# Kernel tuning notes

Measured on AMD Instinct MI355X. Metric: run time of the kernel, lower is better.

## Reference

```python
import jax, jax.numpy as jnp
import numpy as np

B = 32768  # batch of 8x8 boards
DIRS = ((0, 1), (1, 0), (1, 1), (1, -1))  # row, col, main diag, anti diag


def _shift(m, di, dj):
    # out[b,i,j] = m[b,i-di,j-dj], zeros outside the board
    H, W = m.shape[-2], m.shape[-1]
    p = jnp.pad(m, ((0, 0), (max(di, 0), max(-di, 0)), (max(dj, 0), max(-dj, 0))))
    a, b = max(-di, 0), max(-dj, 0)
    return p[:, a:a + H, b:b + W]


def _run_length(m, di, dj):
    # length of the maximal run of ones through each cell along direction (di,dj); 0 where m==0
    left = m
    p = m
    for k in range(1, 8):
        p = p * _shift(m, k * di, k * dj)
        left = left + p
    right = m
    p = m
    for k in range(1, 8):
        p = p * _shift(m, -k * di, -k * dj)
        right = right + p
    return left + right - m


def _conn_channels(m, Ns):
    runs = [_run_length(m, di, dj) for di, dj in DIRS]
    out = []
    for N in Ns:
        c = jnp.zeros(m.shape, dtype=bool)
        for r in runs:
            c = c | (r == N)
        out.append(c.astype(m.dtype))
    return out


def _mark(arr, cond, k0, width):
    u = jnp.broadcast_to(cond[..., None].astype(arr.dtype), cond.shape + (width,))
    return arr.at[..., k0:k0 + width].max(u)


def _line_features(me, op, empty):
    # me/op: [B,R,8] float {0,1}; empty: [B,R,8] bool; lines along last axis
    live2 = jnp.zeros_like(me)
    live3 = jnp.zeros_like(me)
    rush3 = jnp.zeros_like(me)

    def blocked(idx):
        if idx < 0 or idx > 7:  # off-board counts as blocked
            return jnp.ones(me.shape[:-1], dtype=bool)
        return (op[..., idx] > 0) | ((~empty[..., idx]) & (me[..., idx] == 0))

    for k in range(5):  # length-4 windows
        a = ((me[..., k] > 0) & (me[..., k + 1] > 0) & (me[..., k + 2] == 0)
             & (me[..., k + 3] == 0) & empty[..., k + 2] & empty[..., k + 3])
        live2 = _mark(live2, a, k, 2)
        b = ((me[..., k] == 0) & (me[..., k + 1] > 0) & (me[..., k + 2] > 0)
             & (me[..., k + 3] == 0) & empty[..., k] & empty[..., k + 3])
        live2 = _mark(live2, b, k + 1, 2)
    for k in range(4):  # length-5 windows
        open3 = ((me[..., k] == 0) & (me[..., k + 1] > 0) & (me[..., k + 2] > 0)
                 & (me[..., k + 3] > 0) & (me[..., k + 4] == 0))
        c = open3 & empty[..., k] & empty[..., k + 4]
        live3 = _mark(live3, c, k + 1, 3)
        lb, rb = blocked(k - 1), blocked(k + 5)
        d = ((me[..., k] > 0) & (me[..., k + 1] > 0) & (me[..., k + 2] > 0)
             & (me[..., k + 3] == 0) & (me[..., k + 4] == 0) & empty[..., k + 3] & lb)
        rush3 = _mark(rush3, d, k, 3)
        e = open3 & jnp.logical_xor(lb, rb)
        rush3 = _mark(rush3, e, k + 1, 3)
    return live2, live3, rush3


def _live_rush(me, op):
    empty = (me == 0) & (op == 0)
    l2r, l3r, r3r = _line_features(me, op, empty)  # rows
    T = lambda x: jnp.swapaxes(x, 1, 2)
    l2c, l3c, r3c = _line_features(T(me), T(op), T(empty))  # cols
    return (jnp.maximum(l2r, T(l2c)), jnp.maximum(l3r, T(l3c)), jnp.maximum(r3r, T(r3c)))


def _double(x, threshold=2):
    cnt = jnp.sum(x, axis=(1, 2), keepdims=True)
    return (cnt >= threshold).astype(x.dtype) * jnp.ones_like(x)


def setup_inputs() -> dict:
    key = jax.random.key(0)
    k1, _ = jax.random.split(key)
    state = jax.random.randint(k1, (B, 8, 8), 0, 3).astype(jnp.float32) - 1.0  # {-1,0,1}
    side = jnp.ones((B,), dtype=jnp.float32)
    return {"state": state, "side": side}


def reference(state, side):
    s = side[:, None, None]
    my = (state == s).astype(jnp.float32)
    op = (state == -s).astype(jnp.float32)
    feats = [my, op]
    feats += _conn_channels(my, [1, 2, 3])
    feats += _conn_channels(op, [1, 2, 3])
    l2m, l3m, r3m = _live_rush(my, op)
    l2o, l3o, r3o = _live_rush(op, my)
    feats += [l2m, l3m, r3m, _double(l2m, 2), _double(l3m + r3m, 2)]
    feats += [l2o, l3o, r3o, _double(l2o, 2), _double(l3o + r3o, 2)]
    return jnp.stack(feats, axis=1)  # [B, 18, 8, 8]
```

## Files before the change

### kernel.cpp

```cpp
#include <hip/hip_runtime.h>

typedef unsigned long long u64;

#define FILE0 0x0101010101010101ULL
#define NF0   0xFEFEFEFEFEFEFEFEULL
#define NF7   0x7F7F7F7F7F7F7F7FULL

template<int D> __device__ __forceinline__ u64 SH(u64 x) {
  if (D == 0) return (x << 1) & NF0;
  if (D == 1) return x << 8;
  if (D == 2) return (x << 9) & NF0;
  return (x << 7) & NF7;
}
template<int D> __device__ __forceinline__ u64 FW(u64 x) {
  if (D == 0) return (x >> 1) & NF7;
  if (D == 1) return x >> 8;
  if (D == 2) return (x >> 9) & NF7;
  return (x >> 7) & NF0;
}

template<int D> __device__ __forceinline__ void runs(u64 b, u64& r1, u64& r2, u64& r3) {
  u64 f1 = FW<D>(b), f2 = FW<D>(f1), f3 = FW<D>(f2);
  u64 start = b & ~SH<D>(b);
  r1 |= start & ~f1;
  u64 st2 = start & f1 & ~f2;
  r2 |= st2 | SH<D>(st2);
  u64 st3 = start & f1 & f2 & ~f3;
  u64 s3a = SH<D>(st3);
  r3 |= st3 | s3a | SH<D>(s3a);
}

template<int D> __device__ __forceinline__ void linefeat(u64 me, u64 op, u64 empty,
                                                         u64& live2, u64& live3, u64& rush3) {
  const u64 EDGE_LO  = (D == 0) ? FILE0 : 0xFFULL;
  const u64 EDGE_HI3 = (D == 0) ? 0xF8F8F8F8F8F8F8F8ULL
                                : 0xFFFFFFFFFF000000ULL;
  u64 fm1 = FW<D>(me), fm2 = FW<D>(fm1), fm3 = FW<D>(fm2);
  u64 fe1 = FW<D>(empty), fe2 = FW<D>(fe1), fe3 = FW<D>(fe2), fe4 = FW<D>(fe3);
  u64 fn4 = FW<D>(FW<D>(FW<D>(FW<D>(~me))));
  u64 a = me & fm1 & fe2 & fe3;
  live2 |= a | SH<D>(a);
  u64 b = empty & fm1 & fm2 & fe3;
  u64 sb = SH<D>(b);
  live2 |= sb | SH<D>(sb);
  u64 c = empty & fm1 & fm2 & fm3 & fe4;
  u64 sc = SH<D>(c), sc2 = SH<D>(sc);
  live3 |= sc | sc2 | SH<D>(sc2);
  u64 lb  = SH<D>(op) | EDGE_LO;
  u64 fo5 = FW<D>(FW<D>(FW<D>(FW<D>(FW<D>(op)))));
  u64 rb  = fo5 | EDGE_HI3;
  u64 open3 = (~me) & fm1 & fm2 & fm3 & fn4;
  u64 e = open3 & (lb ^ rb);
  u64 se = SH<D>(e), se2 = SH<D>(se);
  rush3 |= se | se2 | SH<D>(se2);
  u64 d = me & fm1 & fm2 & fe3 & fn4 & lb;
  u64 sd = SH<D>(d);
  rush3 |= d | sd | SH<D>(sd);
}

__global__ __launch_bounds__(256) void Agent_56822417326533_kernel(
    const float* __restrict__ state, const float* __restrict__ side,
    float* __restrict__ out, int B) {
  const int lane = threadIdx.x & 63;
  const int wave = blockIdx.x * (blockDim.x >> 6) + (threadIdx.x >> 6);
  const int board0 = wave * 8;
  if (board0 >= B) return;

  u64 my = 0, op = 0;
  const float* sp = state + (size_t)board0 * 64;
  #pragma unroll
  for (int j = 0; j < 8; ++j) {
    if (board0 + j < B) {
      float s = side[board0 + j];
      float v = sp[j * 64 + lane];
      u64 mym = __ballot(v == s);
      u64 opm = __ballot(v == -s);
      if (lane == j) { my = mym; op = opm; }
    }
  }

  u64 empty = ~(my | op);
  u64 ch[18];
  ch[0] = my; ch[1] = op;

  u64 r1m = 0, r2m = 0, r3m = 0, r1o = 0, r2o = 0, r3o = 0;
  runs<0>(my, r1m, r2m, r3m); runs<1>(my, r1m, r2m, r3m);
  runs<2>(my, r1m, r2m, r3m); runs<3>(my, r1m, r2m, r3m);
  runs<0>(op, r1o, r2o, r3o); runs<1>(op, r1o, r2o, r3o);
  runs<2>(op, r1o, r2o, r3o); runs<3>(op, r1o, r2o, r3o);
  ch[2] = r1m; ch[3] = r2m; ch[4] = r3m;
  ch[5] = r1o; ch[6] = r2o; ch[7] = r3o;

  u64 l2m = 0, l3m = 0, ru3m = 0, l2o = 0, l3o = 0, ru3o = 0;
  linefeat<0>(my, op, empty, l2m, l3m, ru3m);
  linefeat<1>(my, op, empty, l2m, l3m, ru3m);
  linefeat<0>(op, my, empty, l2o, l3o, ru3o);
  linefeat<1>(op, my, empty, l2o, l3o, ru3o);
  ch[8] = l2m; ch[9] = l3m; ch[10] = ru3m;
  ch[11] = (__popcll(l2m) >= 2) ? ~0ULL : 0ULL;
  ch[12] = (__popcll(l3m) + __popcll(ru3m) >= 2) ? ~0ULL : 0ULL;
  ch[13] = l2o; ch[14] = l3o; ch[15] = ru3o;
  ch[16] = (__popcll(l2o) >= 2) ? ~0ULL : 0ULL;
  ch[17] = (__popcll(l3o) + __popcll(ru3o) >= 2) ? ~0ULL : 0ULL;

  float* outp = out + (size_t)board0 * 1152 + lane;
  #pragma unroll
  for (int j = 0; j < 8; ++j) {
    if (board0 + j < B) {
      #pragma unroll
      for (int c = 0; c < 18; ++c) {
        u64 m = __shfl(ch[c], j);
        outp[j * 1152 + c * 64] = (float)((m >> lane) & 1ULL);
      }
    }
  }
}

extern "C" void kernel_launch(void* const* d_in, const int* in_sizes, int n_in,
                              void* d_out, int out_size, void* d_ws, size_t ws_size,
                              hipStream_t stream) {
  const float* state = (const float*)d_in[0];
  const float* side  = (const float*)d_in[1];
  float* out = (float*)d_out;
  const int B = in_sizes[0] / 64;
  const int boards_per_block = 32;
  const int blocks = (B + boards_per_block - 1) / boards_per_block;
  hipLaunchKernelGGL(Agent_56822417326533_kernel, dim3(blocks), dim3(256), 0, stream,
                     state, side, out, B);
}
```

Baseline: 159.5 us.

## Process one board per wave and store channels as vectorized float4 writes

Each wave now handles a single board instead of eight. The whole wave computes the bitboard features redundantly, so the per-lane board gather and the 144 shuffles per wave are no longer needed. The output is written with float4 stores (four channels per pass via lane-group selection) plus a float2 tail, which cuts the number of store instructions. In exchange the launch has eight times more waves, and every lane repeats the same scalar bit arithmetic.

```diff
diff --git a/kernel.cpp b/kernel.cpp
--- a/kernel.cpp
+++ b/kernel.cpp
@@ -38,6 +38,7 @@
   u64 fm1 = FW<D>(me), fm2 = FW<D>(fm1), fm3 = FW<D>(fm2);
   u64 fe1 = FW<D>(empty), fe2 = FW<D>(fe1), fe3 = FW<D>(fe2), fe4 = FW<D>(fe3);
   u64 fn4 = FW<D>(FW<D>(FW<D>(FW<D>(~me))));
+  (void)fe1;
   u64 a = me & fm1 & fe2 & fe3;
   live2 |= a | SH<D>(a);
   u64 b = empty & fm1 & fm2 & fe3;
@@ -58,28 +59,25 @@
   rush3 |= d | sd | SH<D>(sd);
 }
 
+__device__ __forceinline__ u64 sel4(int idx, u64 a, u64 b, u64 c, u64 d) {
+  u64 ab = (idx & 1) ? b : a;
+  u64 cd = (idx & 1) ? d : c;
+  return (idx & 2) ? cd : ab;
+}
+
 __global__ __launch_bounds__(256) void Agent_56822417326533_kernel(
     const float* __restrict__ state, const float* __restrict__ side,
     float* __restrict__ out, int B) {
   const int lane = threadIdx.x & 63;
-  const int wave = blockIdx.x * (blockDim.x >> 6) + (threadIdx.x >> 6);
-  const int board0 = wave * 8;
-  if (board0 >= B) return;
+  const int board = blockIdx.x * 4 + (threadIdx.x >> 6);
+  if (board >= B) return;
 
-  u64 my = 0, op = 0;
-  const float* sp = state + (size_t)board0 * 64;
-  #pragma unroll
-  for (int j = 0; j < 8; ++j) {
-    if (board0 + j < B) {
-      float s = side[board0 + j];
-      float v = sp[j * 64 + lane];
-      u64 mym = __ballot(v == s);
-      u64 opm = __ballot(v == -s);
-      if (lane == j) { my = mym; op = opm; }
-    }
-  }
+  const float s = side[board];
+  const float v = state[(size_t)board * 64 + lane];
+  u64 my = __ballot(v == s);
+  u64 op = __ballot(v == -s);
+  u64 empty = ~(my | op);
 
-  u64 empty = ~(my | op);
   u64 ch[18];
   ch[0] = my; ch[1] = op;
 
@@ -103,16 +101,25 @@
   ch[16] = (__popcll(l2o) >= 2) ? ~0ULL : 0ULL;
   ch[17] = (__popcll(l3o) + __popcll(ru3o) >= 2) ? ~0ULL : 0ULL;
 
-  float* outp = out + (size_t)board0 * 1152 + lane;
+  float* outp = out + (size_t)board * 1152;
   #pragma unroll
-  for (int j = 0; j < 8; ++j) {
-    if (board0 + j < B) {
-      #pragma unroll
-      for (int c = 0; c < 18; ++c) {
-        u64 m = __shfl(ch[c], j);
-        outp[j * 1152 + c * 64] = (float)((m >> lane) & 1ULL);
-      }
-    }
+  for (int t = 0; t < 4; ++t) {
+    u64 m = sel4(lane >> 4, ch[4 * t], ch[4 * t + 1], ch[4 * t + 2], ch[4 * t + 3]);
+    unsigned bits = (unsigned)(m >> ((lane & 15) * 4)) & 0xFu;
+    float4 f;
+    f.x = (float)(bits & 1u);
+    f.y = (float)((bits >> 1) & 1u);
+    f.z = (float)((bits >> 2) & 1u);
+    f.w = (float)((bits >> 3) & 1u);
+    *(float4*)(outp + t * 256 + lane * 4) = f;
+  }
+  {
+    u64 m = (lane & 32) ? ch[17] : ch[16];
+    unsigned bits = (unsigned)(m >> ((lane & 31) * 2)) & 0x3u;
+    float2 f;
+    f.x = (float)(bits & 1u);
+    f.y = (float)((bits >> 1) & 1u);
+    *(float2*)(outp + 1024 + lane * 2) = f;
   }
 }
 
@@ -123,8 +130,7 @@
   const float* side  = (const float*)d_in[1];
   float* out = (float*)d_out;
   const int B = in_sizes[0] / 64;
-  const int boards_per_block = 32;
-  const int blocks = (B + boards_per_block - 1) / boards_per_block;
+  const int blocks = (B + 3) / 4;
   hipLaunchKernelGGL(Agent_56822417326533_kernel, dim3(blocks), dim3(256), 0, stream,
                      state, side, out, B);
 }
```

New measurement: 159.0 us. Within noise of the previous version (-0.3%).
